# Kernel optimization log

Hardware: AMD Instinct MI355X
Metric: run time of the kernel (lower is better)

## Reference

```python
import jax, jax.numpy as jnp
import numpy as np

L = 6                      # lmax = mmax (single resolution)
C = 128                    # sphere_channels
H = 256                    # hidden_channels
EC = 128                   # edge_channels
NG = 512                   # gaussian distance basis size
NC = (L + 1) ** 2          # 49 spherical coefficients
GP = 2 * (L + 1) ** 2      # 98 grid points
N_ATOMS = 800
N_EDGES = 8000
MAX_ELEM = 90
CUTOFF = 8.0
M_SIZES = [L - m + 1 for m in range(L + 1)]
MAXIN = L * C              # widest per-m SO2 input (m=1)


def _perm_np():
    # l-primary index of coefficient (l, m) is l*l + l + m
    idx = lambda l, m: l * l + l + m
    p = [idx(l, 0) for l in range(L + 1)]
    for m in range(1, L + 1):
        p += [idx(l, -m) for l in range(m, L + 1)]
        p += [idx(l, m) for l in range(m, L + 1)]
    return np.array(p)

_P = _perm_np()
PERM = jnp.array(_P)          # l-primary -> m-primary (x._m_primary)
INV_PERM = jnp.array(np.argsort(_P))  # m-primary -> l-primary (x._l_primary)


def silu(x):
    return x * jax.nn.sigmoid(x)


def setup_inputs() -> dict:
    key = jax.random.key(0)
    ks = iter(jax.random.split(key, 64))
    def nrm(shape, scale):
        return jax.random.normal(next(ks), shape, dtype=jnp.float32) * np.float32(scale)
    def lin(out_d, in_d):
        return nrm((out_d, in_d), 1.0 / np.sqrt(in_d))
    def so2_params(prefix):
        return {
            prefix + 'w_dist0': lin(H, EC), prefix + 'b_dist0': jnp.zeros((H,), jnp.float32),
            prefix + 'w1_m0': lin(H, M_SIZES[0] * C), prefix + 'w2_m0': lin(M_SIZES[0] * C, H),
            prefix + 'wdist_m': nrm((L, 2 * H, EC), 1.0 / np.sqrt(EC)),
            prefix + 'bdist_m': jnp.zeros((L, 2 * H), jnp.float32),
            prefix + 'w1r': nrm((L, H, MAXIN), 1.0 / np.sqrt(MAXIN)),
            prefix + 'w2r': nrm((L, MAXIN, H), 1.0 / np.sqrt(H)),
            prefix + 'w1i': nrm((L, H, MAXIN), 1.0 / np.sqrt(MAXIN)),
            prefix + 'w2i': nrm((L, MAXIN, H), 1.0 / np.sqrt(H)),
        }
    inp = dict(
        x=nrm((N_ATOMS, NC, C), 1.0),
        edge_distance=jax.random.uniform(next(ks), (N_EDGES,), jnp.float32, 0.5, CUTOFF),
        wigner=nrm((N_EDGES, NC, NC), 1.0 / np.sqrt(NC)),
        wigner_inv=nrm((N_EDGES, NC, NC), 1.0 / np.sqrt(NC)),
        to_grid_mat=nrm((GP, NC), 1.0 / np.sqrt(NC)),
        from_grid_mat=nrm((NC, GP), 1.0 / np.sqrt(GP)),
        w_dist1=lin(EC, NG), b_dist1=jnp.zeros((EC,), jnp.float32),
        src_emb=jax.random.uniform(next(ks), (MAX_ELEM, EC), jnp.float32, -0.001, 0.001),
        tgt_emb=jax.random.uniform(next(ks), (MAX_ELEM, EC), jnp.float32, -0.001, 0.001),
        w_edge1=lin(EC, EC), b_edge1=jnp.zeros((EC,), jnp.float32),
        ws1=lin(C, 2 * C), bs1=jnp.zeros((C,), jnp.float32),
        ws2=lin(C, C), bs2=jnp.zeros((C,), jnp.float32),
        ws3=lin(C, C), bs3=jnp.zeros((C,), jnp.float32),
        atomic_numbers=jax.random.randint(next(ks), (N_ATOMS,), 0, MAX_ELEM),
        edge_index=jax.random.randint(next(ks), (2, N_EDGES), 0, N_ATOMS),
    )
    inp.update(so2_params('s_'))
    inp.update(so2_params('t_'))
    return inp


def _so2_block(xr, x_edge, p):
    # SO2Block: m-primary reorder, m=0 gated MLP, per-m complex gated GEMMs, back to l-primary
    (w_dist0, b_dist0, w1_m0, w2_m0, wdist_m, bdist_m, w1r, w2r, w1i, w2i) = p
    E = xr.shape[0]
    xm = xr[:, PERM]                                   # [E, NC, C] m-primary
    n0 = M_SIZES[0]
    g0 = silu(x_edge @ w_dist0.T + b_dist0)            # [E, H]
    x0 = xm[:, :n0].reshape(E, n0 * C)
    x0 = ((x0 @ w1_m0.T) * g0) @ w2_m0.T
    outs = [x0.reshape(E, n0, C)]
    off = n0
    for m in range(1, L + 1):
        n = M_SIZES[m]; k = n * C
        blk = xm[:, off:off + 2 * n].reshape(E, 2, k)  # [E, 2(real/imag), n*C]
        ge = silu(x_edge @ wdist_m[m - 1].T + bdist_m[m - 1]).reshape(E, 2, H)
        xr_ = jnp.einsum('eik,hk->eih', blk, w1r[m - 1, :, :k]) * ge[:, 0:1]
        xr_ = jnp.einsum('eih,kh->eik', xr_, w2r[m - 1, :k])
        xi_ = jnp.einsum('eik,hk->eih', blk, w1i[m - 1, :, :k]) * ge[:, 1:2]
        xi_ = jnp.einsum('eih,kh->eik', xi_, w2i[m - 1, :k])
        out = jnp.stack([xr_[:, 0] - xi_[:, 1], xr_[:, 1] + xi_[:, 0]], axis=1)
        outs.append(out.reshape(E, 2 * n, C))
        off += 2 * n
    return jnp.concatenate(outs, axis=1)[:, INV_PERM]


def reference(x, edge_distance, wigner, wigner_inv, to_grid_mat, from_grid_mat,
              w_dist1, b_dist1, src_emb, tgt_emb, w_edge1, b_edge1,
              s_w_dist0, s_b_dist0, s_w1_m0, s_w2_m0, s_wdist_m, s_bdist_m,
              s_w1r, s_w2r, s_w1i, s_w2i,
              t_w_dist0, t_b_dist0, t_w1_m0, t_w2_m0, t_wdist_m, t_bdist_m,
              t_w1r, t_w2r, t_w1i, t_w2i,
              ws1, bs1, ws2, bs2, ws3, bs3,
              atomic_numbers, edge_index):
    # --- EdgeBlock ---
    offsets = jnp.linspace(0.0, CUTOFF, NG)
    coeff = np.float32(-0.5 / (CUTOFF / (NG - 1)) ** 2)
    basis = jnp.exp(coeff * (edge_distance[:, None] - offsets) ** 2)   # GaussianSmearing
    x_dist = basis @ w_dist1.T + b_dist1
    x_edge = silu(src_emb[atomic_numbers[edge_index[0]]]
                  + tgt_emb[atomic_numbers[edge_index[1]]] + x_dist)
    x_edge = silu(x_edge @ w_edge1.T + b_edge1)                        # [E, EC]
    # --- gather per-edge embeddings and rotate into edge frame ---
    x_src = jnp.einsum('eij,ejc->eic', wigner, x[edge_index[0]])
    x_tgt = jnp.einsum('eij,ejc->eic', wigner, x[edge_index[1]])
    # --- SO2 blocks ---
    x_src = _so2_block(x_src, x_edge, (s_w_dist0, s_b_dist0, s_w1_m0, s_w2_m0,
                                       s_wdist_m, s_bdist_m, s_w1r, s_w2r, s_w1i, s_w2i))
    x_tgt = _so2_block(x_tgt, x_edge, (t_w_dist0, t_b_dist0, t_w1_m0, t_w2_m0,
                                       t_wdist_m, t_bdist_m, t_w1r, t_w2r, t_w1i, t_w2i))
    msg = x_src + x_tgt
    # --- grid activation (x._grid_act) ---
    g = silu(jnp.einsum('gi,eic->egc', to_grid_mat, msg))
    msg = jnp.einsum('ig,egc->eic', from_grid_mat, g)
    # --- rotate back and aggregate (x._rotate_inv, x._reduce_edge) ---
    msg = jnp.einsum('eij,ejc->eic', wigner_inv, msg)
    x_msg = jax.ops.segment_sum(msg, edge_index[1], num_segments=x.shape[0])
    # --- LayerBlock point-wise spherical nonlinearity on the grid ---
    gx = jnp.einsum('gi,nic->ngc', to_grid_mat, x)
    gm = jnp.einsum('gi,nic->ngc', to_grid_mat, x_msg)
    g = jnp.concatenate([gx, gm], axis=-1)            # [N, GP, 2C]
    g = silu(g @ ws1.T + bs1)
    g = silu(g @ ws2.T + bs2)
    g = g @ ws3.T + bs3
    return jnp.einsum('ig,ngc->nic', from_grid_mat, g)
```

## Files before the change

### kernel.cpp

```cpp
#include <hip/hip_runtime.h>
#include <string.h>

#define EN 8000
#define AN 800

typedef __attribute__((ext_vector_type(8))) short bf16x8;
typedef __attribute__((ext_vector_type(4))) float f32x4;
typedef unsigned short ushort_t;
typedef unsigned int uint32;

__constant__ int c_perm[49] = {
  0,2,6,12,20,30,42,
  1,5,11,19,29,41,
  3,7,13,21,31,43,
  4,10,18,28,40,
  8,14,22,32,44,
  9,17,27,39,
  15,23,33,45,
  16,26,38,
  24,34,46,
  25,37,
  35,47,
  36,
  48
};

__device__ __forceinline__ float siluf(float x) { return x / (1.0f + __expf(-x)); }
__device__ __forceinline__ ushort_t f2bf(float f) {
  uint32 u = __float_as_uint(f);
  u += 0x7fff + ((u >> 16) & 1);
  return (ushort_t)(u >> 16);
}
__device__ __forceinline__ float bf2f(ushort_t h) {
  return __uint_as_float(((uint32)h) << 16);
}
__device__ __forceinline__ void gld16(const void* g, void* l) {
  __builtin_amdgcn_global_load_lds(
      (const __attribute__((address_space(1))) void*)g,
      (__attribute__((address_space(3))) void*)l, 16, 0, 0);
}

__global__ __launch_bounds__(256) void k_build_b2b(
    const float* __restrict__ sw2r, const float* __restrict__ sw2i,
    const float* __restrict__ tw2r, const float* __restrict__ tw2i,
    ushort_t* __restrict__ dst)
{
  long long id = (long long)blockIdx.x * 256 + threadIdx.x;
  if (id >= 5505024LL) return;
  long long base = 0; int m = 1, k = 768;
  for (; m <= 6; ++m) {
    k = (7 - m) * 128;
    long long sz = 2LL * k * 1024;
    if (id < base + sz) break;
    base += sz;
  }
  long long rem = id - base;
  int p = (int)(rem / ((long long)k * 1024));
  int cj = (int)(rem - (long long)p * k * 1024);
  int c = cj >> 10, j = cj & 1023;
  int q = j >> 8, jj = j & 255;
  const float sgn = (q & 1) ? (p ? 1.f : -1.f) : 1.f;
  const float* src = (q < 2) ? (q == 0 ? sw2r : sw2i) : (q == 2 ? tw2r : tw2i);
  dst[id] = f2bf(sgn * src[(long long)(m - 1) * 196608 + c * 256 + jj]);
}

__global__ __launch_bounds__(256) void k_build_bgcat(
    const float* __restrict__ sw0, const float* __restrict__ tw0,
    const float* __restrict__ sw4, const float* __restrict__ tw4,
    const float* __restrict__ sb0, const float* __restrict__ tb0b,
    const float* __restrict__ sbd, const float* __restrict__ tbd,
    ushort_t* __restrict__ w, float* __restrict__ b)
{
  int id = blockIdx.x * 256 + threadIdx.x;
  if (id < 851968) {
    int r = id >> 7, c = id & 127;
    float v;
    if (r < 256) v = sw0[r * 128 + c];
    else if (r < 512) v = tw0[(r - 256) * 128 + c];
    else {
      int rr = r - 512, m = rr >> 10, q = rr & 1023;
      v = (q < 512) ? sw4[m * 65536 + q * 128 + c] : tw4[m * 65536 + (q - 512) * 128 + c];
    }
    w[id] = f2bf(v);
    return;
  }
  id -= 851968;
  if (id < 6656) {
    float v;
    if (id < 256) v = sb0[id];
    else if (id < 512) v = tb0b[id - 256];
    else {
      int rr = id - 512, m = rr >> 10, q = rr & 1023;
      v = (q < 512) ? sbd[m * 512 + q] : tbd[m * 512 + (q - 512)];
    }
    b[id] = v;
  }
}

__global__ __launch_bounds__(256) void k_build_b20b(
    const float* __restrict__ sw3, const float* __restrict__ tw3,
    ushort_t* __restrict__ b20)
{
  int id = blockIdx.x * 256 + threadIdx.x;
  if (id >= 458752) return;
  int cc = id >> 9, j = id & 511;
  b20[id] = f2bf((j < 256) ? sw3[cc * 256 + j] : tw3[cc * 256 + (j - 256)]);
}

__global__ __launch_bounds__(256) void k_build_s1m(
    const float* __restrict__ sw6, const float* __restrict__ sw8,
    const float* __restrict__ tw6, const float* __restrict__ tw8,
    ushort_t* __restrict__ dst)
{
  long long id = (long long)blockIdx.x * 256 + threadIdx.x;
  if (id >= 2752512LL) return;
  long long base = 0; int m = 1, k = 768;
  for (; m <= 6; ++m) {
    k = (7 - m) * 128;
    long long sz = 1024LL * k;
    if (id < base + sz) break;
    base += sz;
  }
  long long rem = id - base;
  int s = (int)(rem / (512LL * k));
  int rr = (int)(rem - (long long)s * 512 * k);
  int r = rr / k, c = rr - r * k;
  const float* src = (r < 256) ? (s ? tw6 : sw6) : (s ? tw8 : sw8);
  int r0 = (r < 256) ? r : r - 256;
  dst[id] = f2bf(src[(long long)(m - 1) * 196608 + r0 * 768 + c]);
}

__global__ __launch_bounds__(256) void k_cvt(
    const float* __restrict__ src, ushort_t* __restrict__ dst, int n)
{
  int id = blockIdx.x * 256 + threadIdx.x;
  if (id < n) dst[id] = f2bf(src[id]);
}

__global__ __launch_bounds__(256) void k_build_tg(
    const float* __restrict__ tg, ushort_t* __restrict__ dst)
{
  int id = blockIdx.x * 256 + threadIdx.x;
  if (id >= 98 * 49) return;
  int r = id / 49, s = id - r * 49;
  dst[id] = f2bf(tg[r * 49 + c_perm[s]]);
}

__global__ __launch_bounds__(256) void k_xT(
    const float* __restrict__ x, ushort_t* __restrict__ xbT)
{
  __shared__ __align__(16) float xs[49 * 128];
  const int a = blockIdx.x, t = threadIdx.x;
  const float4* src = (const float4*)(x + (long long)a * 6272);
  float4* d = (float4*)xs;
  for (int i = t; i < 1568; i += 256) d[i] = src[i];
  __syncthreads();
  ushort_t* o = xbT + (long long)a * 8192;
  int c = t >> 1;
  int jg = (t & 1) << 2;
  #pragma unroll
  for (int u = 0; u < 4; ++u) {
    int g = jg + u;
    bf16x8 v = (bf16x8)0;
    #pragma unroll
    for (int j = 0; j < 8; ++j) {
      int jj = (g << 3) + j;
      if (jj < 49) v[j] = (short)f2bf(xs[jj * 128 + c]);
    }
    *(bf16x8*)&o[(c << 6) + (g << 3)] = v;
  }
}

__global__ __launch_bounds__(256) void k_basis(
    const float* __restrict__ dist, ushort_t* __restrict__ basis)
{
  int id = blockIdx.x * 256 + threadIdx.x;
  if (id >= EN * 512) return;
  int e = id >> 9, g = id & 511;
  const float step = 8.0f / 511.0f;
  const float coeff = -2040.0078125f;
  float df = dist[e] - (float)g * step;
  basis[id] = f2bf(expf(coeff * df * df));
}

__global__ __launch_bounds__(256) void k_emb(
    const float* __restrict__ src_emb, const float* __restrict__ tgt_emb,
    const int* __restrict__ anum, const int* __restrict__ eidx,
    const float* __restrict__ xd, ushort_t* __restrict__ out)
{
  int id = blockIdx.x * 256 + threadIdx.x;
  if (id >= EN * 128) return;
  int e = id >> 7, c = id & 127;
  int a0 = anum[eidx[e]], a1 = anum[eidx[EN + e]];
  out[id] = f2bf(siluf(src_emb[a0 * 128 + c] + tgt_emb[a1 * 128 + c] + xd[id]));
}

__global__ __launch_bounds__(256) void k_rot2(
    const float* __restrict__ wig, const ushort_t* __restrict__ xbT,
    const int* __restrict__ srcl, const int* __restrict__ tgtl,
    ushort_t* __restrict__ osrc, ushort_t* __restrict__ otgt)
{
  __shared__ short Ws[4096];
  __shared__ short Xs[8192];
  __shared__ short Xt[8192];
  const int e = blockIdx.x, tid = threadIdx.x;
  const int lane = tid & 63, wave = tid >> 6;
  const float* wge = wig + (long long)e * 2401;
  #pragma unroll
  for (int t = 0; t < 2; ++t) {
    int ci = (t << 8) + tid;
    int row = ci >> 3, g = ci & 7;
    bf16x8 v = (bf16x8)0;
    if (row < 49) {
      const float* wr = wge + c_perm[row] * 49;
      #pragma unroll
      for (int j = 0; j < 8; ++j) {
        int col = (g << 3) + j;
        if (col < 49) v[j] = (short)f2bf(wr[col]);
      }
    }
    *(bf16x8*)&Ws[(row << 6) + ((g ^ (row & 7)) << 3)] = v;
  }
  const int as = srcl[e], at = tgtl[e];
  const ushort_t* xsg = xbT + (long long)as * 8192;
  const ushort_t* xtg = xbT + (long long)at * 8192;
  #pragma unroll
  for (int t = 0; t < 4; ++t) {
    int ci = (t << 8) + tid;
    int row = ci >> 3, g = ci & 7;
    int ofs = (row << 6) + ((g ^ (row & 7)) << 3);
    *(bf16x8*)&Xs[ofs] = *(const bf16x8*)&xsg[ci << 3];
    *(bf16x8*)&Xt[ofs] = *(const bf16x8*)&xtg[ci << 3];
  }
  __syncthreads();
  const short* Xb = (wave >> 1) ? Xt : Xs;
  ushort_t* ob = ((wave >> 1) ? otgt : osrc) + (long long)e * 6272;
  const int ch = (wave & 1) << 6;
  const int fr = lane & 15, g = lane >> 4;
  f32x4 acc[4][4];
  #pragma unroll
  for (int i = 0; i < 4; ++i)
    #pragma unroll
    for (int j = 0; j < 4; ++j) acc[i][j] = (f32x4){0.f, 0.f, 0.f, 0.f};
  #pragma unroll
  for (int ks = 0; ks < 2; ++ks) {
    bf16x8 af[4], bfv[4];
    int lc = (ks << 2) + g;
    #pragma unroll
    for (int i = 0; i < 4; ++i) {
      int ra = (i << 4) + fr;
      af[i] = *(const bf16x8*)&Ws[(ra << 6) + ((lc ^ (ra & 7)) << 3)];
      int rb = ch + (i << 4) + fr;
      bfv[i] = *(const bf16x8*)&Xb[(rb << 6) + ((lc ^ (rb & 7)) << 3)];
    }
    #pragma unroll
    for (int i = 0; i < 4; ++i)
      #pragma unroll
      for (int j = 0; j < 4; ++j)
        acc[i][j] = __builtin_amdgcn_mfma_f32_16x16x32_bf16(af[i], bfv[j], acc[i][j], 0, 0, 0);
  }
  const int crl = (lane >> 4) << 2, ccl = lane & 15;
  #pragma unroll
  for (int i = 0; i < 4; ++i)
    #pragma unroll
    for (int r = 0; r < 4; ++r) {
      int q = (i << 4) + crl + r;
      if (q < 49) {
        #pragma unroll
        for (int j = 0; j < 4; ++j) {
          int col = ch + (j << 4) + ccl;
          ob[q * 128 + col] = f2bf(acc[i][j][r]);
        }
      }
    }
}

struct GemmP {
  const ushort_t* A; const ushort_t* A2; const ushort_t* B;
  const float* bias; const ushort_t* gate; void* C;
  int a_se, a_si, pair, asplit;
  int ldb;
  int gate_ofs;
  int c_se, c_si, c_ofs;
  int ihalf, act, c_bf16;
  int M, N, K;
  int ngx, wg_base;
};
struct Grouped { GemmP d[14]; int nd; };

__global__ __launch_bounds__(256) void gemm_g(Grouped G) {
  __shared__ short As[8192];
  __shared__ short Bs[8192];
  const int bid = blockIdx.x;
  int di = G.nd - 1;
  for (int i = 1; i < G.nd; ++i) if (bid < G.d[i].wg_base) { di = i - 1; break; }
  const GemmP p = G.d[di];
  const int local = bid - p.wg_base;
  const int bx = local % p.ngx, by = local / p.ngx;
  const int m0 = bx << 7, n0 = by << 7;

  const int tid = threadIdx.x;
  const int lane = tid & 63, wave = tid >> 6;
  const int gl = ((lane & 3) ^ ((lane >> 3) & 3)) << 3;
  const int grow = (wave << 4) + (lane >> 2);
  const int fr = lane & 15, fkg = lane >> 4;
  const int sxor = (fr >> 1) & 3;
  const int wm = (wave >> 1) << 6, wn = (wave & 1) << 6;

  f32x4 acc[4][4];
  #pragma unroll
  for (int i = 0; i < 4; ++i)
    #pragma unroll
    for (int j = 0; j < 4; ++j) acc[i][j] = (f32x4){0.f, 0.f, 0.f, 0.f};

  long long abase;
  {
    int r0 = m0 + grow;
    abase = p.pair
        ? (long long)(r0 >> 1) * p.a_se + (long long)(r0 & 1) * p.a_si
        : (long long)r0 * p.a_se;
  }
  long long abase2;
  {
    int r1 = m0 + 64 + grow;
    abase2 = p.pair
        ? (long long)(r1 >> 1) * p.a_se + (long long)(r1 & 1) * p.a_si
        : (long long)r1 * p.a_se;
  }
  const long long bbase  = (long long)(n0 + grow) * p.ldb;
  const long long bbase2 = (long long)(n0 + 64 + grow) * p.ldb;

  const int nt = p.K >> 5;

  auto STAGE = [&](int buf, int k0) {
    const ushort_t* Ap = p.A;
    int kk = k0;
    if (p.A2 && k0 >= p.asplit) { Ap = p.A2; kk = k0 - p.asplit; }
    const int lofs = (buf << 12) + (wave << 9);
    gld16(Ap + abase + kk + gl,        &As[lofs]);
    gld16(p.B + bbase + k0 + gl,       &Bs[lofs]);
    gld16(Ap + abase2 + kk + gl,       &As[lofs + 2048]);
    gld16(p.B + bbase2 + k0 + gl,      &Bs[lofs + 2048]);
  };

  STAGE(0, 0);
  int cur = 0;
  for (int t = 0; t < nt; ++t) {
    if (t + 1 < nt) {
      STAGE(cur ^ 1, (t + 1) << 5);
      asm volatile("s_waitcnt vmcnt(4)" ::: "memory");
    } else {
      asm volatile("s_waitcnt vmcnt(0)" ::: "memory");
    }
    __builtin_amdgcn_sched_barrier(0);
    __builtin_amdgcn_s_barrier();
    {
      const int bofs = cur << 12;
      bf16x8 af[4], bfv[4];
      #pragma unroll
      for (int i = 0; i < 4; ++i) {
        int ra = wm + (i << 4) + fr;
        int rb = wn + (i << 4) + fr;
        af[i]  = *(const bf16x8*)&As[bofs + (ra << 5) + ((fkg ^ sxor) << 3)];
        bfv[i] = *(const bf16x8*)&Bs[bofs + (rb << 5) + ((fkg ^ sxor) << 3)];
      }
      #pragma unroll
      for (int i = 0; i < 4; ++i)
        #pragma unroll
        for (int j = 0; j < 4; ++j)
          acc[i][j] = __builtin_amdgcn_mfma_f32_16x16x32_bf16(af[i], bfv[j], acc[i][j], 0, 0, 0);
    }
    __builtin_amdgcn_s_barrier();
    cur ^= 1;
  }

  const int crl = (lane >> 4) << 2, ccl = lane & 15;
  #pragma unroll
  for (int mi = 0; mi < 4; ++mi) {
    #pragma unroll
    for (int r = 0; r < 4; ++r) {
      int gr = m0 + wm + mi * 16 + crl + r;
      if (gr >= p.M) continue;
      long long e; int ii;
      if (p.pair) { e = gr >> 1; ii = gr & 1; } else { e = gr; ii = 0; }
      const ushort_t* grw = p.gate ? p.gate + e * 6656 + p.gate_ofs : nullptr;
      #pragma unroll
      for (int ni = 0; ni < 4; ++ni) {
        int gc = n0 + wn + ni * 16 + ccl;
        if (gc >= p.N) continue;
        float v = acc[mi][ni][r];
        if (p.bias) v += p.bias[gc];
        if (p.act)  v = siluf(v);
        if (grw)    v *= bf2f(grw[gc]);
        int par = (p.ihalf && gc >= 256) ? (1 - ii) : ii;
        long long co = e * (long long)p.c_se + (long long)par * p.c_si + p.c_ofs + gc;
        if (p.c_bf16) ((ushort_t*)p.C)[co] = f2bf(v);
        else          ((float*)p.C)[co] = v;
      }
    }
  }
}

struct GridP {
  const float* A; const ushort_t* B; void* C; const float* bias;
  int b_ib, c_ib;
  int M, K, permA, act, c_bf16;
};

#define LDW 40

__global__ __launch_bounds__(256) void gridmm(GridP p) {
  __shared__ short As[128 * LDW];
  __shared__ short Bs[128 * LDW];
  const int e = blockIdx.x;
  const int tid = threadIdx.x;
  const int srow = tid >> 1, sk = (tid & 1) << 4;
  const int lane = tid & 63, wave = tid >> 6;
  const int wm = (wave >> 1) << 6, wn = (wave & 1) << 6;
  const int fr = lane & 15, fk = (lane >> 4) << 3;

  f32x4 acc[4][4];
  #pragma unroll
  for (int i = 0; i < 4; ++i)
    #pragma unroll
    for (int j = 0; j < 4; ++j) acc[i][j] = (f32x4){0.f, 0.f, 0.f, 0.f};

  const ushort_t* bp0 = p.B + (long long)e * p.b_ib;

  for (int k0 = 0; k0 < p.K; k0 += 32) {
    {
      bf16x8 lo = (bf16x8)0, hi = (bf16x8)0;
      if (srow < p.M) {
        const float* ar = p.A + srow * p.K;
        #pragma unroll
        for (int j = 0; j < 8; ++j) {
          int col = k0 + sk + j;
          float v = 0.f;
          if (col < p.K) v = ar[p.permA ? c_perm[col] : col];
          lo[j] = (short)f2bf(v);
        }
        #pragma unroll
        for (int j = 0; j < 8; ++j) {
          int col = k0 + sk + 8 + j;
          float v = 0.f;
          if (col < p.K) v = ar[p.permA ? c_perm[col] : col];
          hi[j] = (short)f2bf(v);
        }
      }
      *(bf16x8*)&As[srow * LDW + sk] = lo;
      *(bf16x8*)&As[srow * LDW + sk + 8] = hi;
    }
    {
      const int c = tid & 127, kq = tid >> 7;
      #pragma unroll
      for (int i = 0; i < 8; ++i) {
        int kk = kq * 16 + i * 2;
        int k1 = k0 + kk, k2 = k1 + 1;
        uint32 v0 = (k1 < p.K) ? (uint32)bp0[(long long)k1 * 128 + c] : 0u;
        uint32 v1 = (k2 < p.K) ? (uint32)bp0[(long long)k2 * 128 + c] : 0u;
        *(uint32*)&Bs[c * LDW + kk] = v0 | (v1 << 16);
      }
    }
    __syncthreads();
    bf16x8 af[4], bfv[4];
    #pragma unroll
    for (int i = 0; i < 4; ++i) {
      af[i]  = *(const bf16x8*)(&As[(wm + i * 16 + fr) * LDW + fk]);
      bfv[i] = *(const bf16x8*)(&Bs[(wn + i * 16 + fr) * LDW + fk]);
    }
    #pragma unroll
    for (int i = 0; i < 4; ++i)
      #pragma unroll
      for (int j = 0; j < 4; ++j)
        acc[i][j] = __builtin_amdgcn_mfma_f32_16x16x32_bf16(af[i], bfv[j], acc[i][j], 0, 0, 0);
    __syncthreads();
  }

  const int crl = (lane >> 4) << 2, ccl = lane & 15;
  #pragma unroll
  for (int mi = 0; mi < 4; ++mi) {
    #pragma unroll
    for (int r = 0; r < 4; ++r) {
      int gr = wm + mi * 16 + crl + r;
      if (gr >= p.M) continue;
      #pragma unroll
      for (int ni = 0; ni < 4; ++ni) {
        int c = wn + ni * 16 + ccl;
        float v = acc[mi][ni][r];
        if (p.bias) v += p.bias[c];
        if (p.act)  v = siluf(v);
        long long co = (long long)e * p.c_ib + gr * 128 + c;
        if (p.c_bf16) ((ushort_t*)p.C)[co] = f2bf(v);
        else          ((float*)p.C)[co] = v;
      }
    }
  }
}

#define SWZ8(cg, r) (((cg) ^ ((r) & 7)) & 7)
#define SWZ16(cg, r) (((cg) & 8) | (((cg) ^ (r)) & 7))

__global__ __launch_bounds__(256, 2) void k_grid(
    const ushort_t* __restrict__ tgb, const ushort_t* __restrict__ fgb,
    const float* __restrict__ wigv, const ushort_t* __restrict__ msgp,
    ushort_t* __restrict__ msg3)
{
  __shared__ short Abuf[8192];
  __shared__ short Bsh[8192];
  __shared__ short Ps[16384];
  const int e = blockIdx.x, tid = threadIdx.x;
  const int lane = tid & 63, wv = tid >> 6;
  const int fr = lane & 15, fk = (lane >> 4) << 3;
  const int crl = (lane >> 4) << 2, ccl = lane & 15;
  const ushort_t* me = msgp + (long long)e * 6272;

  for (int gid = tid; gid < 896; gid += 256) {
    int r = gid >> 3, cg = gid & 7;
    bf16x8 v = (bf16x8)0;
    if (r < 98) {
      #pragma unroll
      for (int j = 0; j < 8; ++j) {
        int col = (cg << 3) + j;
        if (col < 49) v[j] = (short)tgb[r * 49 + col];
      }
    }
    *(bf16x8*)&Abuf[(r << 6) + (SWZ8(cg, r) << 3)] = v;
  }
  for (int gid = tid; gid < 1024; gid += 256) {
    int kg = gid >> 7, c = gid & 127;
    bf16x8 v = (bf16x8)0;
    #pragma unroll
    for (int j = 0; j < 8; ++j) {
      int k = (kg << 3) + j;
      if (k < 49) v[j] = (short)me[k * 128 + c];
    }
    *(bf16x8*)&Bsh[(c << 6) + (SWZ8(kg, c) << 3)] = v;
  }
  {
    int c = tid >> 1, gg = 14 + (tid & 1);
    *(bf16x8*)&Ps[(c << 7) + (SWZ16(gg, c) << 3)] = (bf16x8)0;
  }
  __syncthreads();

  {
    f32x4 acc[7][2];
    #pragma unroll
    for (int i = 0; i < 7; ++i) { acc[i][0] = (f32x4){0,0,0,0}; acc[i][1] = (f32x4){0,0,0,0}; }
    #pragma unroll
    for (int k0 = 0; k0 < 64; k0 += 32) {
      int cg = (k0 + fk) >> 3;
      int br0 = ((2 * wv) << 4) + fr, br1 = ((2 * wv + 1) << 4) + fr;
      bf16x8 bf0 = *(const bf16x8*)&Bsh[(br0 << 6) + (SWZ8(cg, br0) << 3)];
      bf16x8 bf1 = *(const bf16x8*)&Bsh[(br1 << 6) + (SWZ8(cg, br1) << 3)];
      #pragma unroll
      for (int rt = 0; rt < 7; ++rt) {
        int ar = (rt << 4) + fr;
        bf16x8 af = *(const bf16x8*)&Abuf[(ar << 6) + (SWZ8(cg, ar) << 3)];
        acc[rt][0] = __builtin_amdgcn_mfma_f32_16x16x32_bf16(af, bf0, acc[rt][0], 0, 0, 0);
        acc[rt][1] = __builtin_amdgcn_mfma_f32_16x16x32_bf16(af, bf1, acc[rt][1], 0, 0, 0);
      }
    }
    #pragma unroll
    for (int rt = 0; rt < 7; ++rt)
      #pragma unroll
      for (int cj = 0; cj < 2; ++cj) {
        int c = ((2 * wv + cj) << 4) + ccl;
        #pragma unroll
        for (int r = 0; r < 4; ++r) {
          int g = (rt << 4) + crl + r;
          Ps[(c << 7) + (SWZ16(g >> 3, c) << 3) + (g & 7)] =
              (short)f2bf(siluf(acc[rt][cj][r]));
        }
      }
  }
  __syncthreads();
  for (int gid = tid; gid < 1024; gid += 256) {
    int r = gid >> 4, cg = gid & 15;
    bf16x8 v = (bf16x8)0;
    if (r < 49) {
      #pragma unroll
      for (int j = 0; j < 8; ++j) {
        int col = (cg << 3) + j;
        if (col < 98) v[j] = (short)fgb[r * 98 + col];
      }
    }
    *(bf16x8*)&Abuf[(r << 7) + (SWZ16(cg, r) << 3)] = v;
  }
  __syncthreads();

  {
    f32x4 acc[4][2];
    #pragma unroll
    for (int i = 0; i < 4; ++i) { acc[i][0] = (f32x4){0,0,0,0}; acc[i][1] = (f32x4){0,0,0,0}; }
    #pragma unroll
    for (int k0 = 0; k0 < 128; k0 += 32) {
      int cg = (k0 + fk) >> 3;
      int br0 = ((2 * wv) << 4) + fr, br1 = ((2 * wv + 1) << 4) + fr;
      bf16x8 bf0 = *(const bf16x8*)&Ps[(br0 << 7) + (SWZ16(cg, br0) << 3)];
      bf16x8 bf1 = *(const bf16x8*)&Ps[(br1 << 7) + (SWZ16(cg, br1) << 3)];
      #pragma unroll
      for (int rt = 0; rt < 4; ++rt) {
        int ar = (rt << 4) + fr;
        bf16x8 af = *(const bf16x8*)&Abuf[(ar << 7) + (SWZ16(cg, ar) << 3)];
        acc[rt][0] = __builtin_amdgcn_mfma_f32_16x16x32_bf16(af, bf0, acc[rt][0], 0, 0, 0);
        acc[rt][1] = __builtin_amdgcn_mfma_f32_16x16x32_bf16(af, bf1, acc[rt][1], 0, 0, 0);
      }
    }
    #pragma unroll
    for (int rt = 0; rt < 4; ++rt)
      #pragma unroll
      for (int cj = 0; cj < 2; ++cj) {
        int c = ((2 * wv + cj) << 4) + ccl;
        #pragma unroll
        for (int r = 0; r < 4; ++r) {
          int q = (rt << 4) + crl + r;
          Bsh[(c << 6) + (SWZ8(q >> 3, c) << 3) + (q & 7)] = (short)f2bf(acc[rt][cj][r]);
        }
      }
  }
  __syncthreads();
  {
    const float* we = wigv + (long long)e * 2401;
    for (int gid = tid; gid < 512; gid += 256) {
      int r = gid >> 3, cg = gid & 7;
      bf16x8 v = (bf16x8)0;
      if (r < 49) {
        #pragma unroll
        for (int j = 0; j < 8; ++j) {
          int col = (cg << 3) + j;
          if (col < 49) v[j] = (short)f2bf(we[r * 49 + col]);
        }
      }
      *(bf16x8*)&Abuf[(r << 6) + (SWZ8(cg, r) << 3)] = v;
    }
  }
  __syncthreads();

  {
    f32x4 acc[4][2];
    #pragma unroll
    for (int i = 0; i < 4; ++i) { acc[i][0] = (f32x4){0,0,0,0}; acc[i][1] = (f32x4){0,0,0,0}; }
    #pragma unroll
    for (int k0 = 0; k0 < 64; k0 += 32) {
      int cg = (k0 + fk) >> 3;
      int br0 = ((2 * wv) << 4) + fr, br1 = ((2 * wv + 1) << 4) + fr;
      bf16x8 bf0 = *(const bf16x8*)&Bsh[(br0 << 6) + (SWZ8(cg, br0) << 3)];
      bf16x8 bf1 = *(const bf16x8*)&Bsh[(br1 << 6) + (SWZ8(cg, br1) << 3)];
      #pragma unroll
      for (int rt = 0; rt < 4; ++rt) {
        int ar = (rt << 4) + fr;
        bf16x8 af = *(const bf16x8*)&Abuf[(ar << 6) + (SWZ8(cg, ar) << 3)];
        acc[rt][0] = __builtin_amdgcn_mfma_f32_16x16x32_bf16(af, bf0, acc[rt][0], 0, 0, 0);
        acc[rt][1] = __builtin_amdgcn_mfma_f32_16x16x32_bf16(af, bf1, acc[rt][1], 0, 0, 0);
      }
    }
    ushort_t* oe = msg3 + (long long)e * 6272;
    #pragma unroll
    for (int rt = 0; rt < 4; ++rt)
      #pragma unroll
      for (int r = 0; r < 4; ++r) {
        int gi = (rt << 4) + crl + r;
        if (gi < 49) {
          #pragma unroll
          for (int cj = 0; cj < 2; ++cj) {
            int c = ((2 * wv + cj) << 4) + ccl;
            oe[gi * 128 + c] = f2bf(acc[rt][cj][r]);
          }
        }
      }
  }
}

__global__ __launch_bounds__(256) void k_zeroi(int* __restrict__ p, int n) {
  int id = blockIdx.x * 256 + threadIdx.x;
  if (id < n) p[id] = 0;
}

__global__ __launch_bounds__(256) void k_deg(
    const int* __restrict__ tgt, int* __restrict__ deg) {
  int e = blockIdx.x * 256 + threadIdx.x;
  if (e < EN) atomicAdd(&deg[tgt[e]], 1);
}

__global__ __launch_bounds__(1024) void k_prefix(
    const int* __restrict__ deg, int* __restrict__ base) {
  __shared__ int s[1024];
  int t = threadIdx.x;
  s[t] = (t < AN) ? deg[t] : 0;
  __syncthreads();
  for (int ofs = 1; ofs < 1024; ofs <<= 1) {
    int u = (t >= ofs) ? s[t - ofs] : 0;
    __syncthreads();
    s[t] += u;
    __syncthreads();
  }
  if (t < AN) base[t + 1] = s[t];
  if (t == 0) base[0] = 0;
}

__global__ __launch_bounds__(256) void k_fill(
    const int* __restrict__ tgt, const int* __restrict__ base,
    int* __restrict__ list) {
  const int a = blockIdx.x, t = threadIdx.x;
  const int lane = t & 63, w = t >> 6;
  __shared__ int wtot[4];
  __shared__ int runbase;
  if (t == 0) runbase = base[a];
  __syncthreads();
  for (int i0 = 0; i0 < EN; i0 += 256) {
    int e = i0 + t;
    bool m = (e < EN) && (tgt[e] == a);
    unsigned long long bal = __ballot(m);
    if (lane == 0) wtot[w] = __popcll(bal);
    __syncthreads();
    int wbase = 0;
    for (int j = 0; j < w; ++j) wbase += wtot[j];
    int tot = wtot[0] + wtot[1] + wtot[2] + wtot[3];
    if (m) {
      int off = __popcll(bal & ((1ull << lane) - 1ull));
      list[runbase + wbase + off] = e;
    }
    __syncthreads();
    if (t == 0) runbase += tot;
    __syncthreads();
  }
}

__global__ __launch_bounds__(256) void k_gather(
    const ushort_t* __restrict__ msg3, const int* __restrict__ base,
    const int* __restrict__ list, float* __restrict__ xmsg,
    int e0, int ce, int accum)
{
  const int a = blockIdx.x, part = blockIdx.y, t = threadIdx.x;
  const int b0 = base[a], b1 = base[a + 1];
  const int ofs = part * 784;
  float acc[4] = {0.f, 0.f, 0.f, 0.f};
  for (int i = b0; i < b1; ++i) {
    int e = list[i];
    if (e < e0 || e >= e0 + ce) continue;
    const ushort_t* m = msg3 + (long long)(e - e0) * 6272 + ofs;
    #pragma unroll
    for (int u = 0; u < 4; ++u) {
      int idx = t + (u << 8);
      if (idx < 784) acc[u] += bf2f(m[idx]);
    }
  }
  float* o = xmsg + (long long)a * 6272 + ofs;
  #pragma unroll
  for (int u = 0; u < 4; ++u) {
    int idx = t + (u << 8);
    if (idx < 784) {
      if (accum) o[idx] += acc[u]; else o[idx] = acc[u];
    }
  }
}

extern "C" void kernel_launch(void* const* d_in, const int* in_sizes, int n_in,
                              void* d_out, int out_size, void* d_ws, size_t ws_size,
                              hipStream_t stream) {
  const float* x         = (const float*)d_in[0];
  const float* edist     = (const float*)d_in[1];
  const float* wigner    = (const float*)d_in[2];
  const float* wiginv    = (const float*)d_in[3];
  const float* to_grid   = (const float*)d_in[4];
  const float* from_grid = (const float*)d_in[5];
  const float* w_dist1   = (const float*)d_in[6];
  const float* b_dist1   = (const float*)d_in[7];
  const float* src_emb   = (const float*)d_in[8];
  const float* tgt_emb   = (const float*)d_in[9];
  const float* w_edge1   = (const float*)d_in[10];
  const float* b_edge1   = (const float*)d_in[11];
  const float* ws1       = (const float*)d_in[12];
  const float* bs1       = (const float*)d_in[13];
  const float* ws2       = (const float*)d_in[14];
  const float* bs2       = (const float*)d_in[15];
  const float* ws3       = (const float*)d_in[16];
  const float* bs3       = (const float*)d_in[17];
  const int*   anum      = (const int*)d_in[18];
  const int*   eidx      = (const int*)d_in[19];
  const float* sw[10]; const float* tw[10];
  for (int i = 0; i < 10; ++i) {
    sw[i] = (const float*)d_in[20 + i];
    tw[i] = (const float*)d_in[30 + i];
  }
  float* outp = (float*)d_out;

  char* wsb = (char*)d_ws;
  size_t off = 0;
  auto alloc = [&](long long nbytes) {
    char* p = wsb + off; off += (size_t)((nbytes + 63) & ~63LL); return p;
  };
  ushort_t* x_edge  = (ushort_t*)alloc((8000LL + 128) * 128 * 2);
  ushort_t* b2ab    = (ushort_t*)alloc(5505024LL * 2);
  ushort_t* bgcw    = (ushort_t*)alloc(851968LL * 2);
  float*    bgcb    = (float*)alloc(6656 * 4);
  ushort_t* b20b    = (ushort_t*)alloc(458752LL * 2);
  ushort_t* s1m0b   = (ushort_t*)alloc(458752LL * 2);
  ushort_t* s1mb    = (ushort_t*)alloc(2752512LL * 2);
  ushort_t* wd1b    = (ushort_t*)alloc(65536 * 2);
  ushort_t* we1b    = (ushort_t*)alloc(16384 * 2);
  ushort_t* ws1b    = (ushort_t*)alloc(32768 * 2);
  ushort_t* ws2b    = (ushort_t*)alloc(16384 * 2);
  ushort_t* ws3b    = (ushort_t*)alloc(16384 * 2);
  ushort_t* tgb     = (ushort_t*)alloc(4802 * 2);
  ushort_t* fgb     = (ushort_t*)alloc(4802 * 2);
  float*    xmsg    = (float*)alloc(5017600LL * 4);
  ushort_t* xmsgb   = (ushort_t*)alloc((5017600LL + 16384) * 2);
  ushort_t* xb      = (ushort_t*)alloc((5017600LL + 16384) * 2);
  ushort_t* xbT     = (ushort_t*)alloc(6553600LL * 2);
  ushort_t* basis   = (ushort_t*)alloc((8000LL + 128) * 512 * 2);
  float*    x_dist  = (float*)alloc(1024000LL * 4);
  ushort_t* x_distb = (ushort_t*)alloc((8000LL + 128) * 128 * 2);
  int*      deg     = (int*)alloc(800 * 4);
  int*      sbase   = (int*)alloc(801 * 4);
  int*      elist   = (int*)alloc(8000 * 4);
  const size_t fixedB = off;
  char* arena = wsb + off;

  static const int ces[6] = {8000, 4000, 2000, 1000, 500, 250};
  static const int cas[6] = {800, 800, 800, 400, 200, 100};
  int ce = 250, ca = 100;
  for (int i = 0; i < 6; ++i) {
    long long ne = (long long)ces[i] * 76544 + 64LL * 50688;
    long long na = (long long)cas[i] * 87808 + 64LL * 512;
    long long need = (long long)fixedB + (ne > na ? ne : na);
    if (need <= (long long)ws_size) { ce = ces[i]; ca = cas[i]; break; }
  }

  char* ap = arena;
  ushort_t* xrot_s = (ushort_t*)ap;  ap += (long long)(ce + 64) * 12544;
  ushort_t* xrot_t = (ushort_t*)ap;  ap += (long long)(ce + 64) * 12544;
  ushort_t* tb0    = (ushort_t*)ap;  ap += (long long)(ce + 64) * 1024;
  ushort_t* tbm    = (ushort_t*)ap;  ap += (long long)(ce + 64) * 24576;
  ushort_t* msgp   = (ushort_t*)ap;  ap += (long long)ce * 12544;
  ushort_t* gate   = (ushort_t*)ap;
  ushort_t* msg3   = (ushort_t*)arena;
  char* bp = arena;
  ushort_t* hb = (ushort_t*)bp;  bp += (long long)ca * 49 * 256;
  ushort_t* g1 = (ushort_t*)bp;  bp += ((long long)ca * 98 + 64) * 256;
  ushort_t* g2 = (ushort_t*)bp;  bp += ((long long)ca * 98 + 64) * 256;
  ushort_t* g3 = (ushort_t*)bp;

  long long ofs2[7][2], s1ofs[7][2];
  { long long cur = 0, cur1 = 0;
    for (int m = 1; m <= 6; ++m) {
      int k = (7 - m) * 128;
      ofs2[m][0] = cur; cur += (long long)k * 1024;
      ofs2[m][1] = cur; cur += (long long)k * 1024;
      s1ofs[m][0] = cur1; cur1 += 512LL * k;
      s1ofs[m][1] = cur1; cur1 += 512LL * k;
    } }

  auto D0 = []() { GemmP p; memset(&p, 0, sizeof(p)); p.asplit = 1 << 30; return p; };
  auto finalize = [&](Grouped& G) {
    int base = 0;
    for (int i = 0; i < G.nd; ++i) {
      GemmP& p = G.d[i];
      p.ngx = (p.M + 127) >> 7;
      int ngy = (p.N + 127) >> 7;
      p.wg_base = base;
      base += p.ngx * ngy;
    }
    gemm_g<<<base, 256, 0, stream>>>(G);
  };
  auto run1 = [&](GemmP p) { Grouped G; G.d[0] = p; G.nd = 1; finalize(G); };
  auto rungrid = [&](const float* A, int M, int K, int permA,
                     const ushort_t* B, int b_ib, void* C, int c_ib,
                     const float* bias, int act, int c_bf16, int nb) {
    GridP p;
    p.A = A; p.B = B; p.C = C; p.bias = bias;
    p.b_ib = b_ib; p.c_ib = c_ib;
    p.M = M; p.K = K; p.permA = permA; p.act = act; p.c_bf16 = c_bf16;
    gridmm<<<nb, 256, 0, stream>>>(p);
  };
  auto cvt = [&](const float* s, ushort_t* d, int n) {
    k_cvt<<<(n + 255) / 256, 256, 0, stream>>>(s, d, n);
  };

  k_build_b2b<<<(5505024 + 255) / 256, 256, 0, stream>>>(sw[7], sw[9], tw[7], tw[9], b2ab);
  k_build_bgcat<<<(858624 + 255) / 256, 256, 0, stream>>>(
      sw[0], tw[0], sw[4], tw[4], sw[1], tw[1], sw[5], tw[5], bgcw, bgcb);
  k_build_b20b<<<(458752 + 255) / 256, 256, 0, stream>>>(sw[3], tw[3], b20b);
  k_build_s1m<<<(2752512 + 255) / 256, 256, 0, stream>>>(sw[6], sw[8], tw[6], tw[8], s1mb);
  cvt(sw[2], s1m0b, 229376);
  cvt(tw[2], s1m0b + 229376, 229376);
  cvt(w_dist1, wd1b, 65536);
  cvt(w_edge1, we1b, 16384);
  cvt(ws1, ws1b, 32768);
  cvt(ws2, ws2b, 16384);
  cvt(ws3, ws3b, 16384);
  cvt(from_grid, fgb, 4802);
  k_build_tg<<<(4802 + 255) / 256, 256, 0, stream>>>(to_grid, tgb);
  cvt(x, xb, 5017600);
  k_xT<<<AN, 256, 0, stream>>>(x, xbT);

  k_zeroi<<<4, 256, 0, stream>>>(deg, 800);
  k_deg<<<(EN + 255) / 256, 256, 0, stream>>>(eidx + EN, deg);
  k_prefix<<<1, 1024, 0, stream>>>(deg, sbase);
  k_fill<<<AN, 256, 0, stream>>>(eidx + EN, sbase, elist);

  k_basis<<<(EN * 512 + 255) / 256, 256, 0, stream>>>(edist, basis);
  { GemmP p = D0();
    p.A = basis; p.a_se = 512; p.B = wd1b; p.ldb = 512; p.bias = b_dist1;
    p.C = x_dist; p.c_se = 128; p.M = EN; p.N = 128; p.K = 512;
    run1(p); }
  k_emb<<<(EN * 128 + 255) / 256, 256, 0, stream>>>(src_emb, tgt_emb, anum, eidx,
                                                    x_dist, x_distb);
  { GemmP p = D0();
    p.A = x_distb; p.a_se = 128; p.B = we1b; p.ldb = 128; p.bias = b_edge1;
    p.act = 1; p.C = x_edge; p.c_se = 128; p.c_bf16 = 1;
    p.M = EN; p.N = 128; p.K = 128;
    run1(p); }

  static const int offq[7] = {0, 7, 19, 29, 37, 43, 47};

  for (int e0 = 0; e0 < EN; e0 += ce) {
    const int c = ce;
    k_rot2<<<c, 256, 0, stream>>>(wigner + (long long)e0 * 2401, xbT,
                                  eidx + e0, eidx + EN + e0, xrot_s, xrot_t);
    { GemmP p = D0();
      p.A = x_edge + (long long)e0 * 128; p.a_se = 128;
      p.B = bgcw; p.ldb = 128; p.bias = bgcb; p.act = 1;
      p.C = gate; p.c_se = 6656; p.c_bf16 = 1;
      p.M = c; p.N = 6656; p.K = 128;
      run1(p); }
    { Grouped G; G.nd = 14;
      for (int s = 0; s < 2; ++s) {
        GemmP p = D0();
        p.A = s ? xrot_t : xrot_s; p.a_se = 6272;
        p.B = s1m0b + (long long)s * 229376; p.ldb = 896;
        p.gate = gate; p.gate_ofs = s * 256;
        p.C = tb0; p.c_se = 512; p.c_ofs = s * 256; p.c_bf16 = 1;
        p.M = c; p.N = 256; p.K = 896;
        G.d[s] = p;
      }
      int di = 2;
      for (int m = 1; m <= 6; ++m) {
        const int k = (7 - m) * 128, off2 = offq[m];
        for (int s = 0; s < 2; ++s) {
          GemmP p = D0();
          p.A = (s ? xrot_t : xrot_s) + off2 * 128;
          p.a_se = 6272; p.a_si = k; p.pair = 1;
          p.B = s1mb + s1ofs[m][s]; p.ldb = k;
          p.gate = gate; p.gate_ofs = 512 + (m - 1) * 1024 + s * 512;
          p.C = tbm; p.c_se = 12288; p.c_si = 1024;
          p.c_ofs = (m - 1) * 2048 + s * 512;
          p.ihalf = 1; p.c_bf16 = 1;
          p.M = 2 * c; p.N = 512; p.K = k;
          G.d[di++] = p;
        }
      }
      finalize(G); }
    { Grouped G; G.nd = 13;
      { GemmP p = D0();
        p.A = tb0; p.a_se = 512;
        p.B = b20b; p.ldb = 512;
        p.C = msgp; p.c_se = 6272; p.c_bf16 = 1;
        p.M = c; p.N = 896; p.K = 512;
        G.d[0] = p; }
      int di = 1;
      for (int m = 1; m <= 6; ++m) {
        const int n = 7 - m, k = n * 128, off2 = offq[m];
        for (int pp = 0; pp < 2; ++pp) {
          GemmP p = D0();
          p.A = tbm + (m - 1) * 2048 + pp * 1024; p.a_se = 12288;
          p.B = b2ab + ofs2[m][pp]; p.ldb = 1024;
          p.C = msgp; p.c_se = 6272; p.c_ofs = (off2 + (pp ? n : 0)) * 128; p.c_bf16 = 1;
          p.M = c; p.N = k; p.K = 1024;
          G.d[di++] = p;
        }
      }
      finalize(G); }
    k_grid<<<c, 256, 0, stream>>>(tgb, fgb, wiginv + (long long)e0 * 2401, msgp, msg3);
    k_gather<<<dim3(AN, 8), 256, 0, stream>>>(msg3, sbase, elist, xmsg, e0, c, e0 > 0);
  }

  cvt(xmsg, xmsgb, 5017600);

  for (int a0 = 0; a0 < AN; a0 += ca) {
    { GemmP p = D0();
      p.A = xb + (long long)a0 * 6272; p.A2 = xmsgb + (long long)a0 * 6272;
      p.a_se = 128; p.asplit = 128;
      p.B = ws1b; p.ldb = 256;
      p.C = hb; p.c_se = 128; p.c_bf16 = 1;
      p.M = ca * 49; p.N = 128; p.K = 256;
      run1(p); }
    rungrid(to_grid, 98, 49, 0, hb, 6272, g1, 12544, bs1, 1, 1, ca);
    { GemmP p = D0();
      p.A = g1; p.a_se = 128;
      p.B = ws2b; p.ldb = 128; p.bias = bs2; p.act = 1;
      p.C = g2; p.c_se = 128; p.c_bf16 = 1;
      p.M = ca * 98; p.N = 128; p.K = 128;
      run1(p); }
    { GemmP p = D0();
      p.A = g2; p.a_se = 128;
      p.B = ws3b; p.ldb = 128; p.bias = bs3;
      p.C = g3; p.c_se = 128; p.c_bf16 = 1;
      p.M = ca * 98; p.N = 128; p.K = 128;
      run1(p); }
    rungrid(from_grid, 49, 98, 0, g3, 12544, outp + (long long)a0 * 6272, 6272,
            nullptr, 0, 0, ca);
  }
}
```

Baseline: 1.760 ms.

## Stage epilogue outputs through LDS for 16-byte stores, remap blocks per XCD

Epilogues of the rotation kernel, grouped GEMM and grid kernel now write results into swizzled shared memory first, then copy them out with 16-byte vector stores instead of scattered 2-byte stores. The grouped GEMM also remaps block IDs so contiguous tiles land on the same XCD, which should improve L2 locality. The gather kernel now reads 8 bf16 values per thread with fewer blocks. In exchange, extra barriers and LDS traffic are added, and the bf16 GEMM path drops N-bounds checks and applies the gate multiply after bf16 rounding, which slightly changes numerics.

```diff
diff --git a/kernel.cpp b/kernel.cpp
--- a/kernel.cpp
+++ b/kernel.cpp
@@ -234,7 +234,6 @@
   }
   __syncthreads();
   const short* Xb = (wave >> 1) ? Xt : Xs;
-  ushort_t* ob = ((wave >> 1) ? otgt : osrc) + (long long)e * 6272;
   const int ch = (wave & 1) << 6;
   const int fr = lane & 15, g = lane >> 4;
   f32x4 acc[4][4];
@@ -260,6 +259,8 @@
         acc[i][j] = __builtin_amdgcn_mfma_f32_16x16x32_bf16(af[i], bfv[j], acc[i][j], 0, 0, 0);
   }
   const int crl = (lane >> 4) << 2, ccl = lane & 15;
+  __syncthreads();
+  short* Ob = (wave >> 1) ? Xt : Xs;
   #pragma unroll
   for (int i = 0; i < 4; ++i)
     #pragma unroll
@@ -269,10 +270,21 @@
         #pragma unroll
         for (int j = 0; j < 4; ++j) {
           int col = ch + (j << 4) + ccl;
-          ob[q * 128 + col] = f2bf(acc[i][j][r]);
-        }
-      }
-    }
+          Ob[(q << 7) + (((col >> 3) ^ (q & 15)) << 3) + (col & 7)] =
+              (short)f2bf(acc[i][j][r]);
+        }
+      }
+    }
+  __syncthreads();
+  for (int gid = tid; gid < 1568; gid += 256) {
+    int half = gid >= 784;
+    int c784 = half ? gid - 784 : gid;
+    int row = c784 >> 4, cc = c784 & 15;
+    const short* Sb = half ? Xt : Xs;
+    bf16x8 v = *(const bf16x8*)&Sb[(row << 7) + ((cc ^ (row & 15)) << 3)];
+    ushort_t* dst = (half ? otgt : osrc) + (long long)e * 6272 + (row << 7) + (cc << 3);
+    *(bf16x8*)dst = v;
+  }
 }
 
 struct GemmP {
@@ -286,12 +298,19 @@
   int M, N, K;
   int ngx, wg_base;
 };
-struct Grouped { GemmP d[14]; int nd; };
+struct Grouped { GemmP d[14]; int nd; int nwg; };
 
 __global__ __launch_bounds__(256) void gemm_g(Grouped G) {
-  __shared__ short As[8192];
-  __shared__ short Bs[8192];
-  const int bid = blockIdx.x;
+  __shared__ short SH[16384];
+  short* As = SH;
+  short* Bs = SH + 8192;
+  int bid;
+  {
+    int n = G.nwg, orig = blockIdx.x;
+    int q = n >> 3, r = n & 7;
+    int xcd = orig & 7, pos = orig >> 3;
+    bid = (xcd < r ? xcd * (q + 1) : r * (q + 1) + (xcd - r) * q) + pos;
+  }
   int di = G.nd - 1;
   for (int i = 1; i < G.nd; ++i) if (bid < G.d[i].wg_base) { di = i - 1; break; }
   const GemmP p = G.d[di];
@@ -337,10 +356,10 @@
     int kk = k0;
     if (p.A2 && k0 >= p.asplit) { Ap = p.A2; kk = k0 - p.asplit; }
     const int lofs = (buf << 12) + (wave << 9);
-    gld16(Ap + abase + kk + gl,        &As[lofs]);
-    gld16(p.B + bbase + k0 + gl,       &Bs[lofs]);
-    gld16(Ap + abase2 + kk + gl,       &As[lofs + 2048]);
-    gld16(p.B + bbase2 + k0 + gl,      &Bs[lofs + 2048]);
+    gld16(Ap + abase + kk + gl,   &As[lofs]);
+    gld16(p.B + bbase + k0 + gl,  &Bs[lofs]);
+    gld16(Ap + abase2 + kk + gl,  &As[lofs + 2048]);
+    gld16(p.B + bbase2 + k0 + gl, &Bs[lofs + 2048]);
   };
 
   STAGE(0, 0);
@@ -375,27 +394,64 @@
   }
 
   const int crl = (lane >> 4) << 2, ccl = lane & 15;
-  #pragma unroll
-  for (int mi = 0; mi < 4; ++mi) {
-    #pragma unroll
-    for (int r = 0; r < 4; ++r) {
-      int gr = m0 + wm + mi * 16 + crl + r;
-      if (gr >= p.M) continue;
+  if (p.c_bf16) {
+    #pragma unroll
+    for (int mi = 0; mi < 4; ++mi)
+      #pragma unroll
+      for (int r = 0; r < 4; ++r) {
+        int lrow = wm + mi * 16 + crl + r;
+        #pragma unroll
+        for (int ni = 0; ni < 4; ++ni) {
+          int lcol = wn + ni * 16 + ccl;
+          float v = acc[mi][ni][r];
+          int gc = n0 + lcol;
+          if (p.bias) v += p.bias[gc];
+          if (p.act)  v = siluf(v);
+          SH[(lrow << 7) + (((lcol >> 3) ^ (lrow & 15)) << 3) + (lcol & 7)] =
+              (short)f2bf(v);
+        }
+      }
+    __syncthreads();
+    const int lr = tid >> 1, chalf = (tid & 1) << 6;
+    int gr = m0 + lr;
+    if (gr < p.M) {
       long long e; int ii;
       if (p.pair) { e = gr >> 1; ii = gr & 1; } else { e = gr; ii = 0; }
       const ushort_t* grw = p.gate ? p.gate + e * 6656 + p.gate_ofs : nullptr;
       #pragma unroll
-      for (int ni = 0; ni < 4; ++ni) {
-        int gc = n0 + wn + ni * 16 + ccl;
-        if (gc >= p.N) continue;
-        float v = acc[mi][ni][r];
-        if (p.bias) v += p.bias[gc];
-        if (p.act)  v = siluf(v);
-        if (grw)    v *= bf2f(grw[gc]);
+      for (int j = 0; j < 8; ++j) {
+        int lcol = chalf + (j << 3);
+        bf16x8 v = *(const bf16x8*)&SH[(lr << 7) + (((lcol >> 3) ^ (lr & 15)) << 3)];
+        int gc = n0 + lcol;
+        if (grw) {
+          bf16x8 g8 = *(const bf16x8*)&grw[gc];
+          #pragma unroll
+          for (int q2 = 0; q2 < 8; ++q2)
+            v[q2] = (short)f2bf(bf2f((ushort_t)v[q2]) * bf2f((ushort_t)g8[q2]));
+        }
         int par = (p.ihalf && gc >= 256) ? (1 - ii) : ii;
         long long co = e * (long long)p.c_se + (long long)par * p.c_si + p.c_ofs + gc;
-        if (p.c_bf16) ((ushort_t*)p.C)[co] = f2bf(v);
-        else          ((float*)p.C)[co] = v;
+        *(bf16x8*)&((ushort_t*)p.C)[co] = v;
+      }
+    }
+  } else {
+    #pragma unroll
+    for (int mi = 0; mi < 4; ++mi) {
+      #pragma unroll
+      for (int r = 0; r < 4; ++r) {
+        int gr = m0 + wm + mi * 16 + crl + r;
+        if (gr >= p.M) continue;
+        long long e = gr;
+        float* crow = (float*)p.C + e * (long long)p.c_se + p.c_ofs;
+        #pragma unroll
+        for (int ni = 0; ni < 4; ++ni) {
+          int gc = n0 + wn + ni * 16 + ccl;
+          if (gc >= p.N) continue;
+          float v = acc[mi][ni][r];
+          if (p.bias) v += p.bias[gc];
+          if (p.act)  v = siluf(v);
+          crow[gc] = v;
+        }
       }
     }
   }
@@ -654,7 +710,6 @@
         acc[rt][1] = __builtin_amdgcn_mfma_f32_16x16x32_bf16(af, bf1, acc[rt][1], 0, 0, 0);
       }
     }
-    ushort_t* oe = msg3 + (long long)e * 6272;
     #pragma unroll
     for (int rt = 0; rt < 4; ++rt)
       #pragma unroll
@@ -664,10 +719,18 @@
           #pragma unroll
           for (int cj = 0; cj < 2; ++cj) {
             int c = ((2 * wv + cj) << 4) + ccl;
-            oe[gi * 128 + c] = f2bf(acc[rt][cj][r]);
+            Ps[(gi << 7) + (((c >> 3) ^ (gi & 15)) << 3) + (c & 7)] =
+                (short)f2bf(acc[rt][cj][r]);
           }
         }
       }
+    __syncthreads();
+    ushort_t* oe = msg3 + (long long)e * 6272;
+    for (int gid = tid; gid < 784; gid += 256) {
+      int row = gid >> 4, cc = gid & 15;
+      bf16x8 v = *(const bf16x8*)&Ps[(row << 7) + ((cc ^ (row & 15)) << 3)];
+      *(bf16x8*)&oe[(row << 7) + (cc << 3)] = v;
+    }
   }
 }
 
@@ -726,32 +789,34 @@
   }
 }
 
-__global__ __launch_bounds__(256) void k_gather(
+__global__ __launch_bounds__(256) void k_gather4(
     const ushort_t* __restrict__ msg3, const int* __restrict__ base,
     const int* __restrict__ list, float* __restrict__ xmsg,
     int e0, int ce, int accum)
 {
   const int a = blockIdx.x, part = blockIdx.y, t = threadIdx.x;
+  if (t >= 196) return;
   const int b0 = base[a], b1 = base[a + 1];
-  const int ofs = part * 784;
-  float acc[4] = {0.f, 0.f, 0.f, 0.f};
+  const int co = part * 1568 + t * 8;
+  float a8[8];
+  #pragma unroll
+  for (int u = 0; u < 8; ++u) a8[u] = 0.f;
   for (int i = b0; i < b1; ++i) {
     int e = list[i];
     if (e < e0 || e >= e0 + ce) continue;
-    const ushort_t* m = msg3 + (long long)(e - e0) * 6272 + ofs;
-    #pragma unroll
-    for (int u = 0; u < 4; ++u) {
-      int idx = t + (u << 8);
-      if (idx < 784) acc[u] += bf2f(m[idx]);
-    }
-  }
-  float* o = xmsg + (long long)a * 6272 + ofs;
-  #pragma unroll
-  for (int u = 0; u < 4; ++u) {
-    int idx = t + (u << 8);
-    if (idx < 784) {
-      if (accum) o[idx] += acc[u]; else o[idx] = acc[u];
-    }
+    bf16x8 v = *(const bf16x8*)&msg3[(long long)(e - e0) * 6272 + co];
+    #pragma unroll
+    for (int u = 0; u < 8; ++u) a8[u] += bf2f((ushort_t)v[u]);
+  }
+  float* o = xmsg + (long long)a * 6272 + co;
+  if (accum) {
+    #pragma unroll
+    for (int u = 0; u < 8; ++u) o[u] += a8[u];
+  } else {
+    float4 lo = make_float4(a8[0], a8[1], a8[2], a8[3]);
+    float4 hi = make_float4(a8[4], a8[5], a8[6], a8[7]);
+    *(float4*)o = lo;
+    *(float4*)(o + 4) = hi;
   }
 }
 
@@ -861,6 +926,7 @@
       p.wg_base = base;
       base += p.ngx * ngy;
     }
+    G.nwg = base;
     gemm_g<<<base, 256, 0, stream>>>(G);
   };
   auto run1 = [&](GemmP p) { Grouped G; G.d[0] = p; G.nd = 1; finalize(G); };
@@ -972,7 +1038,7 @@
       }
       finalize(G); }
     k_grid<<<c, 256, 0, stream>>>(tgb, fgb, wiginv + (long long)e0 * 2401, msgp, msg3);
-    k_gather<<<dim3(AN, 8), 256, 0, stream>>>(msg3, sbase, elist, xmsg, e0, c, e0 > 0);
+    k_gather4<<<dim3(AN, 4), 256, 0, stream>>>(msg3, sbase, elist, xmsg, e0, c, e0 > 0);
   }
 
   cvt(xmsg, xmsgb, 5017600);
```

New measurement: 1.636 ms. -7.0%, faster.
